# Kernel tuning notes

Measured on AMD Instinct MI355X. Metric: run time of the kernel, lower is better.

## Reference

```python
import jax, jax.numpy as jnp
import numpy as np

S = 3072      # total packed tokens
D = 1536      # hidden_size
H = 12        # num_heads
HD = D // H   # head_dim = 128
NSEQ = 4      # number of packed sequences (images)


def rotate_half(x):
    x1 = x[..., : x.shape[-1] // 2]
    x2 = x[..., x.shape[-1] // 2 :]
    return jnp.concatenate((-x2, x1), axis=-1)


def setup_inputs() -> dict:
    key = jax.random.key(0)
    k1, k2, k3 = jax.random.split(key, 3)
    hidden_states = jax.random.normal(k1, (S, D), jnp.float32)
    # 4 equal-length packed sequences
    cu_seqlens = (jnp.arange(NSEQ + 1, dtype=jnp.int32) * (S // NSEQ))
    # RoPE cos/sin per token, period within each packed sequence
    pos = (jnp.arange(S) % (S // NSEQ)).astype(jnp.float32)
    inv_freq = 1.0 / (10000.0 ** (jnp.arange(0, HD // 2, dtype=jnp.float32) / (HD // 2)))
    freqs = pos[:, None] * inv_freq[None, :]          # [S, HD//2]
    emb = jnp.concatenate([freqs, freqs], axis=-1)    # [S, HD]
    cos, sin = jnp.cos(emb), jnp.sin(emb)
    qkv_w = jax.random.normal(k2, (3 * D, D), jnp.float32) * (D ** -0.5)
    qkv_b = jnp.zeros((3 * D,), jnp.float32)
    proj_w = jax.random.normal(k3, (D, D), jnp.float32) * (D ** -0.5)
    return {
        "hidden_states": hidden_states,
        "cos": cos,
        "sin": sin,
        "qkv_w": qkv_w,
        "qkv_b": qkv_b,
        "proj_w": proj_w,
        "cu_seqlens": cu_seqlens,
    }


def reference(hidden_states, cos, sin, qkv_w, qkv_b, proj_w, cu_seqlens):
    s_len, dim = hidden_states.shape
    # fused QKV projection -> [S, 3, H, HD]
    qkv = (hidden_states @ qkv_w.T + qkv_b).reshape(s_len, 3, H, HD)
    q, k, v = qkv[:, 0], qkv[:, 1], qkv[:, 2]         # each [S, H, HD]
    # inline RoPE (fp32, broadcast over heads)
    c = cos[:, None, :].astype(jnp.float32)
    s = sin[:, None, :].astype(jnp.float32)
    qf, kf = q.astype(jnp.float32), k.astype(jnp.float32)
    q = (qf * c + rotate_half(qf) * s).astype(q.dtype)
    k = (kf * c + rotate_half(kf) * s).astype(k.dtype)
    # block-diagonal (varlen) mask from cu_seqlens
    seg = jnp.searchsorted(cu_seqlens, jnp.arange(s_len), side="right")  # [S]
    same_seq = seg[:, None] == seg[None, :]                              # [S, S]
    bias = jnp.where(same_seq, 0.0, -jnp.inf).astype(jnp.float32)
    scaling = HD ** -0.5
    # scores [H, S, S]
    scores = jnp.einsum("shd,thd->hst", q, k) * scaling + bias[None]
    probs = jax.nn.softmax(scores.astype(jnp.float32), axis=-1).astype(q.dtype)
    attn = jnp.einsum("hst,thd->shd", probs, v).reshape(s_len, dim)
    return attn @ proj_w.T
```

## Files before the change

### kernel.cpp

```cpp
#include <hip/hip_runtime.h>
#include <stdint.h>

#define S_LEN 3072
#define DIM   1536
#define NH    12
#define HD    128
#define QKV_N 4608

typedef unsigned short u16;
typedef __bf16 bf16x8 __attribute__((ext_vector_type(8)));
typedef float  f32x4  __attribute__((ext_vector_type(4)));
typedef u16    u16x8  __attribute__((ext_vector_type(8)));

#define AS1 __attribute__((address_space(1)))
#define AS3 __attribute__((address_space(3)))
#define GLL16(g, l) __builtin_amdgcn_global_load_lds((AS1 void*)(g), (AS3 void*)(l), 16, 0, 0)

__device__ __forceinline__ u16 f2bf(float f) {
  unsigned u = __float_as_uint(f);
  u = (u + 0x7fffu + ((u >> 16) & 1u)) >> 16;
  return (u16)u;
}
__device__ __forceinline__ float bf2f(u16 b) {
  return __uint_as_float(((unsigned)b) << 16);
}

__global__ __launch_bounds__(256) void cvt_bf16(const float* __restrict__ in,
                                                u16* __restrict__ out, int n4) {
  int stride = gridDim.x * blockDim.x;
  for (int i = blockIdx.x * blockDim.x + threadIdx.x; i < n4; i += stride) {
    float4 v = ((const float4*)in)[i];
    ushort4 o;
    o.x = f2bf(v.x); o.y = f2bf(v.y); o.z = f2bf(v.z); o.w = f2bf(v.w);
    ((ushort4*)out)[i] = o;
  }
}


__device__ __forceinline__ bf16x8 frag2(const u16* region, int row, int ch) {
  int L = row >> 1;
  int slot = ((ch + ((row & 1) << 2)) ^ L) & 7;
  return *(const bf16x8*)(region + L * 64 + slot * 8);
}

__global__ __launch_bounds__(512, 2) void gemm_bt_256(const u16* __restrict__ A,
                                                      const u16* __restrict__ B,
                                                      const float* __restrict__ bias,
                                                      u16* __restrict__ Cout,
                                                      int M, int N, int K) {
  __shared__ __attribute__((aligned(16))) u16 lds[8 * 8192];

  const int t = threadIdx.x;
  const int l = t & 63;
  const int w = t >> 6;
  const int wm = w >> 2;
  const int wn = w & 3;
  const int lr = l & 15;
  const int lc = l >> 4;

  const int nbx = N >> 8;
  const int nwg = gridDim.x;
  const int q = nwg >> 3, r = nwg & 7;
  const int xcd = blockIdx.x & 7, rest = blockIdx.x >> 3;
  const int wgid = (xcd < r ? xcd * (q + 1) : r * (q + 1) + (xcd - r) * q) + rest;
  const int m0 = (wgid / nbx) * 256;
  const int n0 = (wgid % nbx) * 256;

  const int nk = K >> 6;

  f32x4 acc[8][4];
  #pragma unroll
  for (int i = 0; i < 8; ++i)
    #pragma unroll
    for (int j = 0; j < 4; ++j) acc[i][j] = f32x4{0.f, 0.f, 0.f, 0.f};

  auto stage_half = [&](int buf, int ks, int ab, int kt) {
    const u16* base = ab ? B : A;
    const int x0 = ab ? n0 : m0;
    u16* dst = lds + (((buf << 2) | (ks << 1) | ab) * 8192);
    #pragma unroll
    for (int i = 0; i < 2; ++i) {
      int C = t + i * 512;
      int L = C >> 3, s = C & 7;
      int u = s ^ (L & 7);
      int row = 2 * L + (u >> 2), ch = u & 3;
      const u16* src = base + (size_t)(x0 + row) * K + kt * 64 + ks * 32 + ch * 8;
      GLL16(src, dst + C * 8);
    }
  };

  stage_half(0, 0, 0, 0); stage_half(0, 0, 1, 0);
  stage_half(0, 1, 0, 0); stage_half(0, 1, 1, 0);
  asm volatile("s_waitcnt vmcnt(4)" ::: "memory");
  __builtin_amdgcn_s_barrier();

  for (int kt = 0; kt < nk; ++kt) {
    const int buf = kt & 1, nbuf = buf ^ 1;
    const bool st = (kt + 1 < nk);

    #pragma unroll
    for (int ks = 0; ks < 2; ++ks) {
      const u16* Ar = lds + (((buf << 2) | (ks << 1) | 0) * 8192);
      const u16* Br = lds + (((buf << 2) | (ks << 1) | 1) * 8192);

      bf16x8 bfrag[4], afr[4];
      #pragma unroll
      for (int ni = 0; ni < 4; ++ni) bfrag[ni] = frag2(Br, wn * 64 + ni * 16 + lr, lc);
      #pragma unroll
      for (int mi = 0; mi < 4; ++mi) afr[mi] = frag2(Ar, wm * 128 + mi * 16 + lr, lc);
      if (st) stage_half(nbuf, ks, 0, kt + 1);
      __builtin_amdgcn_s_barrier();
      __builtin_amdgcn_s_setprio(1);
      #pragma unroll
      for (int mi = 0; mi < 4; ++mi)
        #pragma unroll
        for (int ni = 0; ni < 4; ++ni)
          acc[mi][ni] = __builtin_amdgcn_mfma_f32_16x16x32_bf16(afr[mi], bfrag[ni],
                                                                acc[mi][ni], 0, 0, 0);
      __builtin_amdgcn_s_setprio(0);
      __builtin_amdgcn_s_barrier();

      #pragma unroll
      for (int mi = 0; mi < 4; ++mi)
        afr[mi] = frag2(Ar, wm * 128 + 64 + mi * 16 + lr, lc);
      if (st) {
        stage_half(nbuf, ks, 1, kt + 1);
        asm volatile("s_waitcnt vmcnt(4)" ::: "memory");
      } else {
        asm volatile("s_waitcnt vmcnt(0)" ::: "memory");
      }
      __builtin_amdgcn_s_barrier();
      __builtin_amdgcn_s_setprio(1);
      #pragma unroll
      for (int mi = 0; mi < 4; ++mi)
        #pragma unroll
        for (int ni = 0; ni < 4; ++ni)
          acc[4 + mi][ni] = __builtin_amdgcn_mfma_f32_16x16x32_bf16(afr[mi], bfrag[ni],
                                                                    acc[4 + mi][ni], 0, 0, 0);
      __builtin_amdgcn_s_setprio(0);
      __builtin_amdgcn_s_barrier();
    }
  }

  #pragma unroll
  for (int ni = 0; ni < 4; ++ni) {
    int col = n0 + wn * 64 + ni * 16 + lr;
    float bv = bias ? bias[col] : 0.f;
    #pragma unroll
    for (int mi = 0; mi < 8; ++mi) {
      int rbase = m0 + wm * 128 + mi * 16 + (lc << 2);
      #pragma unroll
      for (int rr = 0; rr < 4; ++rr)
        Cout[(size_t)(rbase + rr) * N + col] = f2bf(acc[mi][ni][rr] + bv);
    }
  }
}

__device__ __forceinline__ bf16x8 lds_frag(const u16* base, int row, int ch) {
  return *(const bf16x8*)(base + row * 64 + ((ch ^ row) & 7) * 8);
}

template <bool BIAS, bool OUTF32>
__global__ __launch_bounds__(256) void gemm_bt(const u16* __restrict__ A,
                                               const u16* __restrict__ B,
                                               const float* __restrict__ bias,
                                               void* __restrict__ Cout,
                                               int M, int N, int K) {
  __shared__ u16 Asm[128 * 64];
  __shared__ u16 Bsm[128 * 64];
  const int t = threadIdx.x;
  const int l = t & 63;
  const int w = t >> 6;
  const int wm = w >> 1, wn = w & 1;
  const int m0 = blockIdx.y * 128, n0 = blockIdx.x * 128;

  f32x4 acc[4][4];
  #pragma unroll
  for (int i = 0; i < 4; ++i)
    #pragma unroll
    for (int j = 0; j < 4; ++j) acc[i][j] = f32x4{0.f, 0.f, 0.f, 0.f};

  for (int k0 = 0; k0 < K; k0 += 64) {
    __syncthreads();
    #pragma unroll
    for (int r4 = 0; r4 < 4; ++r4) {
      int C = t + r4 * 256;
      int row = C >> 3, ch = C & 7;
      int sch = (ch ^ row) & 7;
      GLL16(A + (size_t)(m0 + row) * K + k0 + sch * 8, Asm + (size_t)C * 8);
      GLL16(B + (size_t)(n0 + row) * K + k0 + sch * 8, Bsm + (size_t)C * 8);
    }
    __syncthreads();
    #pragma unroll
    for (int ks = 0; ks < 2; ++ks) {
      bf16x8 af[4], bfr[4];
      #pragma unroll
      for (int mi = 0; mi < 4; ++mi)
        af[mi] = lds_frag(Asm, wm * 64 + mi * 16 + (l & 15), ks * 4 + (l >> 4));
      #pragma unroll
      for (int ni = 0; ni < 4; ++ni)
        bfr[ni] = lds_frag(Bsm, wn * 64 + ni * 16 + (l & 15), ks * 4 + (l >> 4));
      #pragma unroll
      for (int mi = 0; mi < 4; ++mi)
        #pragma unroll
        for (int ni = 0; ni < 4; ++ni)
          acc[mi][ni] = __builtin_amdgcn_mfma_f32_16x16x32_bf16(af[mi], bfr[ni],
                                                                acc[mi][ni], 0, 0, 0);
    }
  }

  #pragma unroll
  for (int ni = 0; ni < 4; ++ni) {
    int col = n0 + wn * 64 + ni * 16 + (l & 15);
    float bv = 0.f;
    if (BIAS) bv = bias[col];
    #pragma unroll
    for (int mi = 0; mi < 4; ++mi) {
      int rbase = m0 + wm * 64 + mi * 16 + ((l >> 4) << 2);
      #pragma unroll
      for (int rr = 0; rr < 4; ++rr) {
        float v = acc[mi][ni][rr] + bv;
        if (OUTF32)
          ((float*)Cout)[(size_t)(rbase + rr) * N + col] = v;
        else
          ((u16*)Cout)[(size_t)(rbase + rr) * N + col] = f2bf(v);
      }
    }
  }
}

__global__ __launch_bounds__(256) void rope_pack(const u16* __restrict__ QKV,
                                                 const float* __restrict__ cosb,
                                                 const float* __restrict__ sinb,
                                                 u16* __restrict__ Qp,
                                                 u16* __restrict__ Kp,
                                                 u16* __restrict__ Vt) {
  __shared__ u16 vtile[64][128];
  const int t = threadIdx.x;
  const int s0 = blockIdx.x * 64;
  const int h = blockIdx.y;

  const int srow = s0 + (t >> 2);
  const int d0 = (t & 3) * 16;
  const u16* qkvrow = QKV + (size_t)srow * QKV_N + h * HD;
  const float qscale = 0.08838834764831845f * 1.4426950408889634f;
  #pragma unroll
  for (int which = 0; which < 2; ++which) {
    const u16* src = qkvrow + which * DIM;
    u16* dst = (which ? Kp : Qp) + ((size_t)h * S_LEN + srow) * HD;
    const float sc = which ? 1.f : qscale;
    #pragma unroll
    for (int j = 0; j < 16; ++j) {
      int d = d0 + j;
      float xlo = bf2f(src[d]);
      float xhi = bf2f(src[d + 64]);
      float clo = cosb[srow * HD + d], chi = cosb[srow * HD + d + 64];
      float slo = sinb[srow * HD + d], shi = sinb[srow * HD + d + 64];
      dst[d]      = f2bf((xlo * clo - xhi * slo) * sc);
      dst[d + 64] = f2bf((xhi * chi + xlo * shi) * sc);
    }
  }

  #pragma unroll
  for (int r4 = 0; r4 < 4; ++r4) {
    int C = t + r4 * 256;
    int row = C >> 4, ch = C & 15;
    *(uint4*)(&vtile[row][ch * 8]) =
        *(const uint4*)(QKV + (size_t)(s0 + row) * QKV_N + 2 * DIM + h * HD + ch * 8);
  }
  __syncthreads();
  const int d = t >> 1;
  const int sc0 = (t & 1) * 32;
  u16* vdst = Vt + ((size_t)h * HD + d) * S_LEN + s0 + sc0;
  #pragma unroll
  for (int j = 0; j < 32; j += 8) {
    u16x8 v;
    #pragma unroll
    for (int e = 0; e < 8; ++e) v[e] = vtile[sc0 + j + e][d];
    *(u16x8*)(vdst + j) = v;
  }
}

__global__ __launch_bounds__(256) void attn_fwd(const u16* __restrict__ Qp,
                                                const u16* __restrict__ Kp,
                                                const u16* __restrict__ Vt,
                                                const int* __restrict__ cu,
                                                u16* __restrict__ Obf) {
  __shared__ u16 K_lds[64 * 128];
  __shared__ u16 VT_lds[128 * 64];
  __shared__ u16 P_lds[4][16 * 72];

  const int t = threadIdx.x;
  const int l = t & 63;
  const int w = t >> 6;
  const int q0 = blockIdx.x * 64;
  const int h = blockIdx.y;

  int cs = 0, ce = S_LEN;
  #pragma unroll
  for (int b = 0; b < 4; ++b) {
    int lo = cu[b], hi = cu[b + 1];
    if (q0 >= lo && q0 < hi) { cs = lo; ce = hi; }
  }

  const int qrow = q0 + w * 16 + (l & 15);
  bf16x8 qf[4];
  const u16* qptr = Qp + ((size_t)h * S_LEN + qrow) * HD + ((l >> 4) * 8);
  #pragma unroll
  for (int ks = 0; ks < 4; ++ks) qf[ks] = *(const bf16x8*)(qptr + ks * 32);

  f32x4 acc_o[8];
  #pragma unroll
  for (int i = 0; i < 8; ++i) acc_o[i] = f32x4{0.f, 0.f, 0.f, 0.f};
  float m_run[4], l_run[4];
  #pragma unroll
  for (int r = 0; r < 4; ++r) { m_run[r] = -1e30f; l_run[r] = 0.f; }

  for (int kv0 = cs; kv0 < ce; kv0 += 64) {
    __syncthreads();
    {
      const u16* kbase = Kp + ((size_t)h * S_LEN + kv0) * HD;
      #pragma unroll
      for (int r4 = 0; r4 < 4; ++r4) {
        int C = t + r4 * 256;
        int row = C >> 4, ch = C & 15;
        int sch = (ch & 8) | ((ch ^ row) & 7);
        GLL16(kbase + row * HD + sch * 8, K_lds + (size_t)C * 8);
      }
      const u16* vbase = Vt + (size_t)h * HD * S_LEN + kv0;
      #pragma unroll
      for (int r4 = 0; r4 < 4; ++r4) {
        int C = t + r4 * 256;
        int row = C >> 3, ch = C & 7;
        int sch = (ch ^ row) & 7;
        GLL16(vbase + (size_t)row * S_LEN + sch * 8, VT_lds + (size_t)C * 8);
      }
    }
    __syncthreads();

    f32x4 s_acc[4];
    #pragma unroll
    for (int nf = 0; nf < 4; ++nf) {
      s_acc[nf] = f32x4{0.f, 0.f, 0.f, 0.f};
      int kcol = nf * 16 + (l & 15);
      #pragma unroll
      for (int ks = 0; ks < 4; ++ks) {
        int ch = ks * 4 + (l >> 4);
        int sch = (ch & 8) | ((ch ^ kcol) & 7);
        bf16x8 kf = *(const bf16x8*)(K_lds + kcol * 128 + sch * 8);
        s_acc[nf] = __builtin_amdgcn_mfma_f32_16x16x32_bf16(qf[ks], kf, s_acc[nf], 0, 0, 0);
      }
    }

    float p[4][4], alpha[4];
    #pragma unroll
    for (int r = 0; r < 4; ++r) {
      float v = fmaxf(fmaxf(s_acc[0][r], s_acc[1][r]), fmaxf(s_acc[2][r], s_acc[3][r]));
      #pragma unroll
      for (int m = 1; m < 16; m <<= 1) v = fmaxf(v, __shfl_xor(v, m, 64));
      float mn = fmaxf(m_run[r], v);
      alpha[r] = __builtin_amdgcn_exp2f(m_run[r] - mn);
      m_run[r] = mn;
      float sum = 0.f;
      #pragma unroll
      for (int nf = 0; nf < 4; ++nf) {
        float pv = __builtin_amdgcn_exp2f(s_acc[nf][r] - mn);
        p[nf][r] = pv;
        sum += pv;
      }
      #pragma unroll
      for (int m = 1; m < 16; m <<= 1) sum += __shfl_xor(sum, m, 64);
      l_run[r] = l_run[r] * alpha[r] + sum;
    }
    #pragma unroll
    for (int onf = 0; onf < 8; ++onf)
      #pragma unroll
      for (int r = 0; r < 4; ++r) acc_o[onf][r] *= alpha[r];

    u16* pl = P_lds[w];
    #pragma unroll
    for (int nf = 0; nf < 4; ++nf)
      #pragma unroll
      for (int r = 0; r < 4; ++r)
        pl[((l >> 4) * 4 + r) * 72 + nf * 16 + (l & 15)] = f2bf(p[nf][r]);

    #pragma unroll
    for (int ks = 0; ks < 2; ++ks) {
      bf16x8 pa = *(const bf16x8*)(pl + (l & 15) * 72 + ks * 32 + (l >> 4) * 8);
      #pragma unroll
      for (int onf = 0; onf < 8; ++onf) {
        int d = onf * 16 + (l & 15);
        int ch = ks * 4 + (l >> 4);
        int sch = (ch ^ d) & 7;
        bf16x8 vf = *(const bf16x8*)(VT_lds + d * 64 + sch * 8);
        acc_o[onf] = __builtin_amdgcn_mfma_f32_16x16x32_bf16(pa, vf, acc_o[onf], 0, 0, 0);
      }
    }
  }

  #pragma unroll
  for (int r = 0; r < 4; ++r) {
    float inv = 1.f / l_run[r];
    int srow = q0 + w * 16 + ((l >> 4) << 2) + r;
    u16* orow = Obf + (size_t)srow * DIM + h * HD + (l & 15);
    #pragma unroll
    for (int onf = 0; onf < 8; ++onf) orow[onf * 16] = f2bf(acc_o[onf][r] * inv);
  }
}

extern "C" void kernel_launch(void* const* d_in, const int* in_sizes, int n_in,
                              void* d_out, int out_size, void* d_ws, size_t ws_size,
                              hipStream_t stream) {
  const float* hidden = (const float*)d_in[0];
  const float* cosb   = (const float*)d_in[1];
  const float* sinb   = (const float*)d_in[2];
  const float* qkv_w  = (const float*)d_in[3];
  const float* qkv_b  = (const float*)d_in[4];
  const float* proj_w = (const float*)d_in[5];
  const int*   cu     = (const int*)d_in[6];

  u16* Hbf   = (u16*)d_ws;
  u16* Wqkv  = Hbf   + (size_t)S_LEN * DIM;
  u16* Wproj = Wqkv  + (size_t)QKV_N * DIM;
  u16* QKVbf = Wproj + (size_t)DIM * DIM;
  u16* Kp    = QKVbf + (size_t)S_LEN * QKV_N;
  u16* Vt    = Kp    + (size_t)NH * S_LEN * HD;
  u16* Qp    = Wqkv;
  u16* Abf   = Hbf;

  cvt_bf16<<<2048, 256, 0, stream>>>(hidden, Hbf, S_LEN * DIM / 4);
  cvt_bf16<<<2048, 256, 0, stream>>>(qkv_w, Wqkv, QKV_N * DIM / 4);
  cvt_bf16<<<2048, 256, 0, stream>>>(proj_w, Wproj, DIM * DIM / 4);

  gemm_bt_256<<<(S_LEN / 256) * (QKV_N / 256), 512, 0, stream>>>(
      Hbf, Wqkv, qkv_b, QKVbf, S_LEN, QKV_N, DIM);

  rope_pack<<<dim3(S_LEN / 64, NH), 256, 0, stream>>>(QKVbf, cosb, sinb, Qp, Kp, Vt);

  attn_fwd<<<dim3(S_LEN / 64, NH), 256, 0, stream>>>(Qp, Kp, Vt, cu, Abf);

  gemm_bt<false, true><<<dim3(DIM / 128, S_LEN / 128), 256, 0, stream>>>(
      Abf, Wproj, nullptr, d_out, S_LEN, DIM, DIM);
}
```

Before: 172.6 us.

## Deepen QKV GEMM prefetch pipeline and merge three bf16 conversion launches

The QKV GEMM main loop now processes both k-halves of a tile explicitly and issues the next loads earlier: k-half 1 of tile kt+1 and k-half 0 of tile kt+2 go into the buffer just consumed. This increases how far global-to-LDS loads run ahead of the MFMA work, to hide memory latency. The three fp32-to-bf16 conversion kernels are also merged into one launch to cut launch overhead. The reworked vmcnt wait logic and buffer reuse are delicate and could introduce stalls or LDS race hazards.

```diff
diff --git a/kernel.cpp b/kernel.cpp
--- a/kernel.cpp
+++ b/kernel.cpp
@@ -25,14 +25,20 @@
   return __uint_as_float(((unsigned)b) << 16);
 }
 
-__global__ __launch_bounds__(256) void cvt_bf16(const float* __restrict__ in,
-                                                u16* __restrict__ out, int n4) {
+__global__ __launch_bounds__(256) void cvt_bf16_3(const float* __restrict__ in0, u16* __restrict__ out0, int n0,
+                                                  const float* __restrict__ in1, u16* __restrict__ out1, int n1,
+                                                  const float* __restrict__ in2, u16* __restrict__ out2, int n2) {
+  int total = n0 + n1 + n2;
   int stride = gridDim.x * blockDim.x;
-  for (int i = blockIdx.x * blockDim.x + threadIdx.x; i < n4; i += stride) {
-    float4 v = ((const float4*)in)[i];
+  for (int i = blockIdx.x * blockDim.x + threadIdx.x; i < total; i += stride) {
+    const float* src; u16* dst; int j;
+    if (i < n0)           { src = in0; dst = out0; j = i; }
+    else if (i < n0 + n1) { src = in1; dst = out1; j = i - n0; }
+    else                  { src = in2; dst = out2; j = i - n0 - n1; }
+    float4 v = ((const float4*)src)[j];
     ushort4 o;
     o.x = f2bf(v.x); o.y = f2bf(v.y); o.z = f2bf(v.z); o.w = f2bf(v.w);
-    ((ushort4*)out)[i] = o;
+    ((ushort4*)dst)[j] = o;
   }
 }
 
@@ -91,55 +97,86 @@
 
   stage_half(0, 0, 0, 0); stage_half(0, 0, 1, 0);
   stage_half(0, 1, 0, 0); stage_half(0, 1, 1, 0);
+  if (nk > 1) { stage_half(1, 0, 0, 1); stage_half(1, 0, 1, 1); }
   asm volatile("s_waitcnt vmcnt(4)" ::: "memory");
   __builtin_amdgcn_s_barrier();
 
   for (int kt = 0; kt < nk; ++kt) {
     const int buf = kt & 1, nbuf = buf ^ 1;
-    const bool st = (kt + 1 < nk);
-
-    #pragma unroll
-    for (int ks = 0; ks < 2; ++ks) {
-      const u16* Ar = lds + (((buf << 2) | (ks << 1) | 0) * 8192);
-      const u16* Br = lds + (((buf << 2) | (ks << 1) | 1) * 8192);
-
-      bf16x8 bfrag[4], afr[4];
-      #pragma unroll
-      for (int ni = 0; ni < 4; ++ni) bfrag[ni] = frag2(Br, wn * 64 + ni * 16 + lr, lc);
-      #pragma unroll
-      for (int mi = 0; mi < 4; ++mi) afr[mi] = frag2(Ar, wm * 128 + mi * 16 + lr, lc);
-      if (st) stage_half(nbuf, ks, 0, kt + 1);
-      __builtin_amdgcn_s_barrier();
-      __builtin_amdgcn_s_setprio(1);
-      #pragma unroll
-      for (int mi = 0; mi < 4; ++mi)
-        #pragma unroll
-        for (int ni = 0; ni < 4; ++ni)
-          acc[mi][ni] = __builtin_amdgcn_mfma_f32_16x16x32_bf16(afr[mi], bfrag[ni],
-                                                                acc[mi][ni], 0, 0, 0);
-      __builtin_amdgcn_s_setprio(0);
-      __builtin_amdgcn_s_barrier();
-
-      #pragma unroll
-      for (int mi = 0; mi < 4; ++mi)
-        afr[mi] = frag2(Ar, wm * 128 + 64 + mi * 16 + lr, lc);
-      if (st) {
-        stage_half(nbuf, ks, 1, kt + 1);
-        asm volatile("s_waitcnt vmcnt(4)" ::: "memory");
-      } else {
-        asm volatile("s_waitcnt vmcnt(0)" ::: "memory");
-      }
-      __builtin_amdgcn_s_barrier();
-      __builtin_amdgcn_s_setprio(1);
-      #pragma unroll
-      for (int mi = 0; mi < 4; ++mi)
-        #pragma unroll
-        for (int ni = 0; ni < 4; ++ni)
-          acc[4 + mi][ni] = __builtin_amdgcn_mfma_f32_16x16x32_bf16(afr[mi], bfrag[ni],
-                                                                    acc[4 + mi][ni], 0, 0, 0);
-      __builtin_amdgcn_s_setprio(0);
-      __builtin_amdgcn_s_barrier();
-    }
+    const bool st1 = (kt + 1 < nk);
+    const bool st2 = (kt + 2 < nk);
+
+    const u16* A0 = lds + (((buf << 2) | 0) * 8192);
+    const u16* B0 = lds + (((buf << 2) | 1) * 8192);
+    const u16* A1 = lds + (((buf << 2) | 2) * 8192);
+    const u16* B1 = lds + (((buf << 2) | 3) * 8192);
+
+    bf16x8 bfrag[4], afr[4];
+
+    #pragma unroll
+    for (int ni = 0; ni < 4; ++ni) bfrag[ni] = frag2(B0, wn * 64 + ni * 16 + lr, lc);
+    #pragma unroll
+    for (int mi = 0; mi < 4; ++mi) afr[mi] = frag2(A0, wm * 128 + mi * 16 + lr, lc);
+    if (st1) stage_half(nbuf, 1, 0, kt + 1);
+    __builtin_amdgcn_s_barrier();
+    __builtin_amdgcn_s_setprio(1);
+    #pragma unroll
+    for (int mi = 0; mi < 4; ++mi)
+      #pragma unroll
+      for (int ni = 0; ni < 4; ++ni)
+        acc[mi][ni] = __builtin_amdgcn_mfma_f32_16x16x32_bf16(afr[mi], bfrag[ni],
+                                                              acc[mi][ni], 0, 0, 0);
+    __builtin_amdgcn_s_setprio(0);
+    __builtin_amdgcn_s_barrier();
+
+    #pragma unroll
+    for (int mi = 0; mi < 4; ++mi) afr[mi] = frag2(A0, wm * 128 + 64 + mi * 16 + lr, lc);
+    if (st1) stage_half(nbuf, 1, 1, kt + 1);
+    __builtin_amdgcn_s_barrier();
+    __builtin_amdgcn_s_setprio(1);
+    #pragma unroll
+    for (int mi = 0; mi < 4; ++mi)
+      #pragma unroll
+      for (int ni = 0; ni < 4; ++ni)
+        acc[4 + mi][ni] = __builtin_amdgcn_mfma_f32_16x16x32_bf16(afr[mi], bfrag[ni],
+                                                                  acc[4 + mi][ni], 0, 0, 0);
+    __builtin_amdgcn_s_setprio(0);
+    __builtin_amdgcn_s_barrier();
+
+    #pragma unroll
+    for (int ni = 0; ni < 4; ++ni) bfrag[ni] = frag2(B1, wn * 64 + ni * 16 + lr, lc);
+    #pragma unroll
+    for (int mi = 0; mi < 4; ++mi) afr[mi] = frag2(A1, wm * 128 + mi * 16 + lr, lc);
+    if (st2) stage_half(buf, 0, 0, kt + 2);
+    __builtin_amdgcn_s_barrier();
+    __builtin_amdgcn_s_setprio(1);
+    #pragma unroll
+    for (int mi = 0; mi < 4; ++mi)
+      #pragma unroll
+      for (int ni = 0; ni < 4; ++ni)
+        acc[mi][ni] = __builtin_amdgcn_mfma_f32_16x16x32_bf16(afr[mi], bfrag[ni],
+                                                              acc[mi][ni], 0, 0, 0);
+    __builtin_amdgcn_s_setprio(0);
+    __builtin_amdgcn_s_barrier();
+
+    #pragma unroll
+    for (int mi = 0; mi < 4; ++mi) afr[mi] = frag2(A1, wm * 128 + 64 + mi * 16 + lr, lc);
+    if (st2) {
+      stage_half(buf, 0, 1, kt + 2);
+      asm volatile("s_waitcnt vmcnt(4)" ::: "memory");
+    } else if (st1) {
+      asm volatile("s_waitcnt vmcnt(0)" ::: "memory");
+    }
+    __builtin_amdgcn_s_barrier();
+    __builtin_amdgcn_s_setprio(1);
+    #pragma unroll
+    for (int mi = 0; mi < 4; ++mi)
+      #pragma unroll
+      for (int ni = 0; ni < 4; ++ni)
+        acc[4 + mi][ni] = __builtin_amdgcn_mfma_f32_16x16x32_bf16(afr[mi], bfrag[ni],
+                                                                  acc[4 + mi][ni], 0, 0, 0);
+    __builtin_amdgcn_s_setprio(0);
+    __builtin_amdgcn_s_barrier();
   }
 
   #pragma unroll
@@ -428,9 +465,9 @@
   u16* Qp    = Wqkv;
   u16* Abf   = Hbf;
 
-  cvt_bf16<<<2048, 256, 0, stream>>>(hidden, Hbf, S_LEN * DIM / 4);
-  cvt_bf16<<<2048, 256, 0, stream>>>(qkv_w, Wqkv, QKV_N * DIM / 4);
-  cvt_bf16<<<2048, 256, 0, stream>>>(proj_w, Wproj, DIM * DIM / 4);
+  cvt_bf16_3<<<2048, 256, 0, stream>>>(hidden, Hbf, S_LEN * DIM / 4,
+                                       qkv_w, Wqkv, QKV_N * DIM / 4,
+                                       proj_w, Wproj, DIM * DIM / 4);
 
   gemm_bt_256<<<(S_LEN / 256) * (QKV_N / 256), 512, 0, stream>>>(
       Hbf, Wqkv, qkv_b, QKVbf, S_LEN, QKV_N, DIM);
```

New measurement: 169.7 us. No clear change (-1.7%).
